# Performance work log

Hardware: AMD Instinct MI355X
Metric: run time of the kernel (lower is better)

Reference implementation:

```python
import jax, jax.numpy as jnp
import numpy as np

B, D, H, E, K = 8192, 1024, 4096, 8, 2
LOSS_COEF = 0.01
EPS_COMBINE = float(np.finfo(np.float64).eps)  # np.finfo(float).eps used in combine


def setup_inputs() -> dict:
    key = jax.random.key(0)
    ks = jax.random.split(key, 6)
    s_in = 1.0 / np.sqrt(D)
    s_hid = 1.0 / np.sqrt(H)
    return {
        "x": jax.random.normal(ks[0], (B, D), jnp.float32),
        "w_gate": jax.random.uniform(ks[1], (E, D), jnp.float32, -s_in, s_in),
        "fc1_w": jax.random.uniform(ks[2], (E, H, D), jnp.float32, -s_in, s_in),
        "fc1_b": jax.random.uniform(ks[3], (E, H), jnp.float32, -s_in, s_in),
        "fc2_w": jax.random.uniform(ks[4], (E, D, H), jnp.float32, -s_hid, s_hid),
        "fc2_b": jax.random.uniform(ks[5], (E, D), jnp.float32, -s_hid, s_hid),
    }


def _cv_squared(v):
    # torch .var() uses ddof=1
    return jnp.var(v, ddof=1) / (jnp.mean(v) ** 2 + 1e-10)


def _top_k_gating(x, w_gate):
    # clean logits (noisy_gating=False): [B, E]
    logits = x @ w_gate.T
    top_vals, top_idx = jax.lax.top_k(logits, K + 1)  # min(k+1, E)
    topk_vals = top_vals[:, :K]
    topk_idx = top_idx[:, :K]
    topk_gates = jax.nn.softmax(topk_vals, axis=1)
    gates = jnp.zeros((x.shape[0], E), x.dtype)
    gates = gates.at[jnp.arange(x.shape[0])[:, None], topk_idx].set(topk_gates)
    return gates


def _forward(x, w_gate, fc1_w, fc1_b, fc2_w, fc2_b):
    gates = _top_k_gating(x, w_gate)            # [B, E], sparse (k nonzeros/row)
    importance = gates.sum(axis=0)              # [E]
    load = (gates > 0).sum(axis=0).astype(jnp.float32)
    loss = (_cv_squared(importance) + _cv_squared(load)) * LOSS_COEF

    # Dense-equivalent expert compute: tokens with gate==0 contribute 0 to the
    # combine, identical math to SparseDispatcher's gather/scatter.
    h = jnp.einsum('bd,ehd->beh', x, fc1_w) + fc1_b            # [B, E, H]
    h = jax.nn.gelu(h, approximate=False)                      # torch exact gelu
    o = jnp.einsum('beh,edh->bed', h, fc2_w) + fc2_b           # [B, E, D]
    log_p = jax.nn.log_softmax(o, axis=-1)                     # LogSoftmax(dim=1)

    # combine: exp, weight by gates, scatter-add, eps-fill, log
    combined = jnp.einsum('be,bed->bd', gates, jnp.exp(log_p)) # [B, D]
    combined = jnp.where(combined == 0, EPS_COMBINE, combined)
    y = jnp.log(combined)
    return y, loss


def reference(x, w_gate, fc1_w, fc1_b, fc2_w, fc2_b):
    return _forward(x, w_gate, fc1_w, fc1_b, fc2_w, fc2_b)
```

## Files before the change

kernel.cpp:

```cpp
#include <hip/hip_runtime.h>
#include <cstdint>
#include <cmath>

#define BT 8192
#define DD 1024
#define HH 4096
#define EE 8

typedef __attribute__((ext_vector_type(8))) short short8;
typedef __attribute__((ext_vector_type(4))) float f32x4;
typedef unsigned short u16;
typedef unsigned int u32;

__device__ __forceinline__ u16 f2bf(float f) {
    u32 u = __float_as_uint(f);
    u += 0x7FFFu + ((u >> 16) & 1u);
    return (u16)(u >> 16);
}

__device__ __forceinline__ void gld_lds16(const void* g, void* l) {
    __builtin_amdgcn_global_load_lds((__attribute__((address_space(1))) void*)g,
                                     (__attribute__((address_space(3))) void*)l,
                                     16, 0, 0);
}

__global__ void cvt_kernel(const float* __restrict__ src, u16* __restrict__ dst, int n8) {
    int i = blockIdx.x * blockDim.x + threadIdx.x;
    if (i >= n8) return;
    size_t base = (size_t)i * 8;
    float4 a = *(const float4*)(src + base);
    float4 b = *(const float4*)(src + base + 4);
    uint4 o;
    o.x = (u32)f2bf(a.x) | ((u32)f2bf(a.y) << 16);
    o.y = (u32)f2bf(a.z) | ((u32)f2bf(a.w) << 16);
    o.z = (u32)f2bf(b.x) | ((u32)f2bf(b.y) << 16);
    o.w = (u32)f2bf(b.z) | ((u32)f2bf(b.w) << 16);
    *(uint4*)(dst + base) = o;
}

__global__ void gating_kernel(const float* __restrict__ x, const float* __restrict__ wg,
                              float* __restrict__ gate_arr, int* __restrict__ list,
                              int* __restrict__ info,
                              int* __restrict__ counts, float* __restrict__ importance) {
    int wave = (blockIdx.x * blockDim.x + threadIdx.x) >> 6;
    int lane = threadIdx.x & 63;
    if (wave >= BT) return;
    const float* xr = x + (size_t)wave * DD;
    double acc[EE];
#pragma unroll
    for (int e = 0; e < EE; ++e) acc[e] = 0.0;
    for (int i = lane; i < DD; i += 64) {
        double xv = (double)xr[i];
#pragma unroll
        for (int e = 0; e < EE; ++e)
            acc[e] += xv * (double)wg[e * DD + i];
    }
#pragma unroll
    for (int e = 0; e < EE; ++e) {
        double v = acc[e];
        for (int off = 32; off; off >>= 1) v += __shfl_down(v, off, 64);
        acc[e] = v;
    }
    if (lane == 0) {
        int i0 = 0; double v0 = acc[0];
        for (int e = 1; e < EE; ++e) if (acc[e] > v0) { v0 = acc[e]; i0 = e; }
        int i1 = -1; double v1 = -1e300;
        for (int e = 0; e < EE; ++e) { if (e == i0) continue; if (acc[e] > v1) { v1 = acc[e]; i1 = e; } }
        double e1 = exp(v1 - v0);
        double s = 1.0 + e1;
        float g0 = (float)(1.0 / s);
        float g1 = (float)(e1 / s);
        gate_arr[2 * wave]     = g0;
        gate_arr[2 * wave + 1] = g1;
        atomicAdd(&importance[i0], g0);
        atomicAdd(&importance[i1], g1);
        int p0 = atomicAdd(&counts[i0], 1);
        list[i0 * BT + p0] = wave;
        int p1 = atomicAdd(&counts[i1], 1);
        list[i1 * BT + p1] = wave;
        info[2 * wave]     = (i0 << 16) | p0;
        info[2 * wave + 1] = (i1 << 16) | p1;
    }
}

__global__ void loss_kernel(const int* __restrict__ counts, const float* __restrict__ importance,
                            int* __restrict__ offs, float* __restrict__ out_loss) {
    if (threadIdx.x == 0 && blockIdx.x == 0) {
        double mi = 0, ml = 0;
        int off = 0;
        for (int e = 0; e < EE; e++) {
            offs[e] = off; off += counts[e];
            mi += (double)importance[e]; ml += (double)counts[e];
        }
        mi /= EE; ml /= EE;
        double vi = 0, vl = 0;
        for (int e = 0; e < EE; e++) {
            double di = (double)importance[e] - mi; vi += di * di;
            double dl = (double)counts[e] - ml;     vl += dl * dl;
        }
        vi /= (EE - 1); vl /= (EE - 1);
        double cv_i = vi / (mi * mi + 1e-10);
        double cv_l = vl / (ml * ml + 1e-10);
        *out_loss = (float)((cv_i + cv_l) * 0.01);
    }
}

__global__ void gather_x_kernel(const float* __restrict__ x, const int* __restrict__ list,
                                const int* __restrict__ counts, const int* __restrict__ offs,
                                u16* __restrict__ xg) {
    int r = blockIdx.x;
    int e = 0;
#pragma unroll
    for (int i = 1; i < EE; ++i) if (r >= offs[i]) e = i;
    int m = r - offs[e];
    if (m >= counts[e]) return;
    int token = list[e * BT + m];
    const float* src = x + (size_t)token * DD;
    u16* dst = xg + (size_t)r * DD;
    int i = threadIdx.x * 4;
    float4 a = *(const float4*)(src + i);
    uint2 o;
    o.x = (u32)f2bf(a.x) | ((u32)f2bf(a.y) << 16);
    o.y = (u32)f2bf(a.z) | ((u32)f2bf(a.w) << 16);
    *(uint2*)(dst + i) = o;
}

template <int K, int NT, bool GELU>
__global__ __launch_bounds__(256) void moe_gemm(const u16* __restrict__ Asrc,
                                                const u16* __restrict__ Bsrc,
                                                const float* __restrict__ bias,
                                                const int* __restrict__ counts,
                                                const int* __restrict__ offs,
                                                u16* __restrict__ outB,
                                                float* __restrict__ outF) {
    const int e = blockIdx.x & 7;
    const int slot = blockIdx.x >> 3;
    const int slots = gridDim.x >> 3;
    const int cnt = counts[e];
    const int mt = (cnt + 127) >> 7;
    const int work = mt * (NT / 128);
    const int ebase = offs[e];

    const int tid = threadIdx.x;
    const int lane = tid & 63;
    const int wv = tid >> 6;
    const int myrow = tid & 127;
    const int kch = tid >> 7;
    const int moff = (wv >> 1) * 64;
    const int noff = (wv & 1) * 64;
    const int kq = lane >> 4;
    const int rsub = lane & 15;
    const int rq = (lane >> 4) * 4;

    __shared__ u16 As[128 * 32];
    __shared__ u16 Bs[128 * 32];

    for (int w = slot; w < work; w += slots) {
        const int ntile = w / mt;
        const int mtile = w - ntile * mt;
        const int mbase = mtile * 128;
        const int nbase = ntile * 128;
        const int mmax = cnt - mbase;
        const int rowbase = ebase + mbase;

        const size_t arow = (size_t)(rowbase + min(myrow, mmax - 1));
        const u16* aptr = Asrc + arow * (size_t)K + kch * 8;
        const u16* bptr = Bsrc + ((size_t)e * NT + nbase + myrow) * (size_t)K + kch * 8;

        f32x4 acc[4][4] = {};
        for (int k0 = 0; k0 < K; k0 += 32) {
            gld_lds16(aptr + k0,      &As[tid * 8]);
            gld_lds16(aptr + k0 + 16, &As[(tid + 256) * 8]);
            gld_lds16(bptr + k0,      &Bs[tid * 8]);
            gld_lds16(bptr + k0 + 16, &Bs[(tid + 256) * 8]);
            __syncthreads();
            short8 af[4], bfr[4];
#pragma unroll
            for (int mi = 0; mi < 4; mi++)
                af[mi] = *(const short8*)&As[(kq * 128 + moff + mi * 16 + rsub) * 8];
#pragma unroll
            for (int ni = 0; ni < 4; ni++)
                bfr[ni] = *(const short8*)&Bs[(kq * 128 + noff + ni * 16 + rsub) * 8];
#pragma unroll
            for (int mi = 0; mi < 4; mi++)
#pragma unroll
                for (int ni = 0; ni < 4; ni++)
                    acc[mi][ni] = __builtin_amdgcn_mfma_f32_16x16x32_bf16(af[mi], bfr[ni], acc[mi][ni], 0, 0, 0);
            __syncthreads();
        }

        float bvals[4];
#pragma unroll
        for (int ni = 0; ni < 4; ni++)
            bvals[ni] = bias[(size_t)e * NT + nbase + noff + ni * 16 + rsub];
#pragma unroll
        for (int mi = 0; mi < 4; mi++) {
#pragma unroll
            for (int r = 0; r < 4; r++) {
                int m = moff + mi * 16 + rq + r;
                if (m < mmax) {
                    size_t ro = (size_t)(rowbase + m);
#pragma unroll
                    for (int ni = 0; ni < 4; ni++) {
                        int n = nbase + noff + ni * 16 + rsub;
                        float v = acc[mi][ni][r] + bvals[ni];
                        if constexpr (GELU) {
                            v = 0.5f * v * (1.0f + erff(v * 0.7071067811865476f));
                            outB[ro * NT + n] = f2bf(v);
                        } else {
                            outF[ro * NT + n] = v;
                        }
                    }
                }
            }
        }
    }
}

__global__ void combine_kernel(const float* __restrict__ o, const float* __restrict__ gates,
                               const int* __restrict__ info, const int* __restrict__ offs,
                               float* __restrict__ y) {
    const int b = blockIdx.x;
    const int tid = threadIdx.x;
    const int lane = tid & 63, wv = tid >> 6;
    const int inf0 = info[2 * b], inf1 = info[2 * b + 1];
    const int r0i = offs[inf0 >> 16] + (inf0 & 0xffff);
    const int r1i = offs[inf1 >> 16] + (inf1 & 0xffff);
    const float* r0 = o + (size_t)r0i * DD;
    const float* r1 = o + (size_t)r1i * DD;
    float v0[4], v1[4];
#pragma unroll
    for (int j = 0; j < 4; j++) { v0[j] = r0[tid + 256 * j]; v1[j] = r1[tid + 256 * j]; }
    float m0 = fmaxf(fmaxf(v0[0], v0[1]), fmaxf(v0[2], v0[3]));
    float m1 = fmaxf(fmaxf(v1[0], v1[1]), fmaxf(v1[2], v1[3]));
#pragma unroll
    for (int off = 32; off; off >>= 1) {
        m0 = fmaxf(m0, __shfl_xor(m0, off, 64));
        m1 = fmaxf(m1, __shfl_xor(m1, off, 64));
    }
    __shared__ float sred[2][4];
    if (lane == 0) { sred[0][wv] = m0; sred[1][wv] = m1; }
    __syncthreads();
    m0 = fmaxf(fmaxf(sred[0][0], sred[0][1]), fmaxf(sred[0][2], sred[0][3]));
    m1 = fmaxf(fmaxf(sred[1][0], sred[1][1]), fmaxf(sred[1][2], sred[1][3]));
    float p0[4], p1[4], s0 = 0.f, s1 = 0.f;
#pragma unroll
    for (int j = 0; j < 4; j++) {
        p0[j] = expf(v0[j] - m0); s0 += p0[j];
        p1[j] = expf(v1[j] - m1); s1 += p1[j];
    }
#pragma unroll
    for (int off = 32; off; off >>= 1) {
        s0 += __shfl_xor(s0, off, 64);
        s1 += __shfl_xor(s1, off, 64);
    }
    __shared__ float sred2[2][4];
    if (lane == 0) { sred2[0][wv] = s0; sred2[1][wv] = s1; }
    __syncthreads();
    s0 = sred2[0][0] + sred2[0][1] + sred2[0][2] + sred2[0][3];
    s1 = sred2[1][0] + sred2[1][1] + sred2[1][2] + sred2[1][3];
    const float c0 = gates[2 * b] / s0;
    const float c1 = gates[2 * b + 1] / s1;
#pragma unroll
    for (int j = 0; j < 4; j++) {
        float c = p0[j] * c0 + p1[j] * c1;
        if (c == 0.f) c = 2.2204460492503131e-16f;
        y[(size_t)b * DD + tid + 256 * j] = logf(c);
    }
}

extern "C" void kernel_launch(void* const* d_in, const int* in_sizes, int n_in,
                              void* d_out, int out_size, void* d_ws, size_t ws_size,
                              hipStream_t stream) {
    const float* x     = (const float*)d_in[0];
    const float* wgate = (const float*)d_in[1];
    const float* fc1w  = (const float*)d_in[2];
    const float* fc1b  = (const float*)d_in[3];
    const float* fc2w  = (const float*)d_in[4];
    const float* fc2b  = (const float*)d_in[5];
    float* out = (float*)d_out;

    char* ws = (char*)d_ws;
    const size_t MB = 1024 * 1024;
    u16* w1b = (u16*)(ws);
    float* o = (float*)(ws);
    u16* w2b = (u16*)(ws + 64 * MB);
    u16* h   = (u16*)(ws + 128 * MB);
    u16* xg  = (u16*)(ws + 256 * MB);
    char* meta = ws + 288 * MB;
    int* counts       = (int*)meta;
    int* offs         = (int*)(meta + 32);
    float* importance = (float*)(meta + 64);
    float* gate_arr   = (float*)(meta + 128);
    int* info         = (int*)(meta + 128 + 65536);
    int* list         = (int*)(meta + 128 + 131072);

    hipMemsetAsync(meta, 0, 96, stream);
    cvt_kernel<<<(EE * HH * DD / 8 + 255) / 256, 256, 0, stream>>>(fc1w, w1b, EE * HH * DD / 8);
    cvt_kernel<<<(EE * DD * HH / 8 + 255) / 256, 256, 0, stream>>>(fc2w, w2b, EE * DD * HH / 8);
    gating_kernel<<<BT / 4, 256, 0, stream>>>(x, wgate, gate_arr, list, info, counts, importance);
    loss_kernel<<<1, 64, 0, stream>>>(counts, importance, offs, out + (size_t)BT * DD);
    gather_x_kernel<<<2 * BT, 256, 0, stream>>>(x, list, counts, offs, xg);

    moe_gemm<DD, HH, true><<<8 * 544, 256, 0, stream>>>(
        xg, w1b, fc1b, counts, offs, h, nullptr);
    moe_gemm<HH, DD, false><<<8 * 136, 256, 0, stream>>>(
        h, w2b, fc2b, counts, offs, nullptr, o);
    combine_kernel<<<BT, 256, 0, stream>>>(o, gate_arr, info, offs, out);
}
```

Measured before the change: 1.409 ms.

## Double-buffer LDS tiles with 64-wide K step in expert GEMM

Switches the expert GEMM main loop from single-buffered 32-wide K tiles to double-buffered 64-wide K tiles. The global-to-LDS loads for the next tile are issued before the current tile is computed, so memory latency overlaps with MFMA work, and there is one barrier per 64 K instead of two per 32 K. The cost is four times the LDS per block (64 KB), which may reduce occupancy, and it relies on the barrier waiting for the outstanding async LDS loads.

```diff
diff --git a/kernel.cpp b/kernel.cpp
--- a/kernel.cpp
+++ b/kernel.cpp
@@ -152,8 +152,10 @@
     const int rsub = lane & 15;
     const int rq = (lane >> 4) * 4;
 
-    __shared__ u16 As[128 * 32];
-    __shared__ u16 Bs[128 * 32];
+    __shared__ u16 As[2][128 * 64];
+    __shared__ u16 Bs[2][128 * 64];
+
+    constexpr int NK = K / 64;
 
     for (int w = slot; w < work; w += slots) {
         const int ntile = w / mt;
@@ -167,26 +169,43 @@
         const u16* aptr = Asrc + arow * (size_t)K + kch * 8;
         const u16* bptr = Bsrc + ((size_t)e * NT + nbase + myrow) * (size_t)K + kch * 8;
 
+#pragma unroll
+        for (int j = 0; j < 4; j++) {
+            gld_lds16(aptr + j * 16, &As[0][(tid + 256 * j) * 8]);
+            gld_lds16(bptr + j * 16, &Bs[0][(tid + 256 * j) * 8]);
+        }
+
         f32x4 acc[4][4] = {};
-        for (int k0 = 0; k0 < K; k0 += 32) {
-            gld_lds16(aptr + k0,      &As[tid * 8]);
-            gld_lds16(aptr + k0 + 16, &As[(tid + 256) * 8]);
-            gld_lds16(bptr + k0,      &Bs[tid * 8]);
-            gld_lds16(bptr + k0 + 16, &Bs[(tid + 256) * 8]);
+        for (int k = 0; k < NK; k++) {
             __syncthreads();
-            short8 af[4], bfr[4];
-#pragma unroll
-            for (int mi = 0; mi < 4; mi++)
-                af[mi] = *(const short8*)&As[(kq * 128 + moff + mi * 16 + rsub) * 8];
-#pragma unroll
-            for (int ni = 0; ni < 4; ni++)
-                bfr[ni] = *(const short8*)&Bs[(kq * 128 + noff + ni * 16 + rsub) * 8];
-#pragma unroll
-            for (int mi = 0; mi < 4; mi++)
+            if (k + 1 < NK) {
+                const u16* an = aptr + (k + 1) * 64;
+                const u16* bn = bptr + (k + 1) * 64;
+                const int nb = (k + 1) & 1;
+#pragma unroll
+                for (int j = 0; j < 4; j++) {
+                    gld_lds16(an + j * 16, &As[nb][(tid + 256 * j) * 8]);
+                    gld_lds16(bn + j * 16, &Bs[nb][(tid + 256 * j) * 8]);
+                }
+            }
+            const int cb = k & 1;
+#pragma unroll
+            for (int kk = 0; kk < 2; kk++) {
+                const u16* Ab = &As[cb][(kk * 4 + kq) * 1024];
+                const u16* Bb = &Bs[cb][(kk * 4 + kq) * 1024];
+                short8 af[4], bfr[4];
+#pragma unroll
+                for (int mi = 0; mi < 4; mi++)
+                    af[mi] = *(const short8*)&Ab[(moff + mi * 16 + rsub) * 8];
 #pragma unroll
                 for (int ni = 0; ni < 4; ni++)
-                    acc[mi][ni] = __builtin_amdgcn_mfma_f32_16x16x32_bf16(af[mi], bfr[ni], acc[mi][ni], 0, 0, 0);
-            __syncthreads();
+                    bfr[ni] = *(const short8*)&Bb[(noff + ni * 16 + rsub) * 8];
+#pragma unroll
+                for (int mi = 0; mi < 4; mi++)
+#pragma unroll
+                    for (int ni = 0; ni < 4; ni++)
+                        acc[mi][ni] = __builtin_amdgcn_mfma_f32_16x16x32_bf16(af[mi], bfr[ni], acc[mi][ni], 0, 0, 0);
+            }
         }
 
         float bvals[4];
```

Measured after the change: 1.494 ms. +6.0%, slower.
